# Optimization experiments

Measured on AMD Instinct MI355X. Metric: run time of the kernel, lower is better.

Reference implementation:

```python
import jax, jax.numpy as jnp
import numpy as np

N_NODES = 100000
N_EDGES = 1600000
NFEAT, NHID, NCLASS = 64, 128, 32


def _glorot(key, shape):
    fan_in, fan_out = shape[0], shape[1]
    lim = np.sqrt(6.0 / (fan_in + fan_out))
    return jax.random.uniform(key, shape, jnp.float32, -lim, lim)


def setup_inputs() -> dict:
    key = jax.random.key(0)
    ks = jax.random.split(key, 12)
    x = jax.random.normal(ks[0], (N_NODES, NFEAT), jnp.float32)
    edge_idx = jax.random.randint(ks[1], (2, N_EDGES), 0, N_NODES, jnp.int64)
    edge_weight = jax.random.uniform(ks[2], (N_EDGES,), jnp.float32)
    return {
        "x": x,
        "edge_idx": edge_idx,
        "edge_weight": edge_weight,
        # SAGEConv 1: out = mean_agg(x) @ Wl1 + b1 + x @ Wr1
        "Wl1": _glorot(ks[3], (NFEAT, NHID)),
        "Wr1": _glorot(ks[4], (NFEAT, NHID)),
        "b1": jnp.zeros((NHID,), jnp.float32),
        # SAGEConv 2
        "Wl2": _glorot(ks[5], (NHID, NHID)),
        "Wr2": _glorot(ks[6], (NHID, NHID)),
        "b2": jnp.zeros((NHID,), jnp.float32),
        # fc head: Linear(nhid, nclass) -> Linear(nclass, 1)
        "Wfc1": _glorot(ks[7], (NHID, NCLASS)),
        "bfc1": jnp.zeros((NCLASS,), jnp.float32),
        "Wfc2": _glorot(ks[8], (NCLASS, 1)),
        "bfc2": jnp.zeros((1,), jnp.float32),
    }


def _sage_conv(x, src, dst, Wl, Wr, b, n_nodes):
    # mean aggregation of source features at destination nodes
    msg_sum = jax.ops.segment_sum(x[src], dst, num_segments=n_nodes)  # [N, d]
    deg = jax.ops.segment_sum(jnp.ones((src.shape[0], 1), x.dtype), dst,
                              num_segments=n_nodes)                    # [N, 1]
    mean = msg_sum / jnp.maximum(deg, 1.0)
    return mean @ Wl + b + x @ Wr


def reference(x, edge_idx, edge_weight, Wl1, Wr1, b1, Wl2, Wr2, b2,
              Wfc1, bfc1, Wfc2, bfc2):
    n_nodes = x.shape[0]
    src, dst = edge_idx[0], edge_idx[1]
    # dropout is identity in eval mode (training=False)
    h = _sage_conv(x, src, dst, Wl1, Wr1, b1, n_nodes)   # [N, nhid]
    h = _sage_conv(h, src, dst, Wl2, Wr2, b2, n_nodes)   # [N, nhid]
    h = h @ Wfc1 + bfc1                                   # [N, nclass]
    out = h @ Wfc2 + bfc2                                 # [N, 1]
    return out
```

## Files before the change

kernel.cpp:

```cpp
#include <hip/hip_runtime.h>

#define S_SHIFT 8
#define S_NODES 256
#define NBKT    400
#define CAP     5120
#define CHUNK   8192
#define NREP    8
#define FTH     512
#define NDOTS   160

__global__ __launch_bounds__(FTH) void fused_kernel(
    const float* __restrict__ x,
    const int* __restrict__ src, const int* __restrict__ dst,
    int E, int N, int B, int nscat,
    int* __restrict__ cursor, unsigned* __restrict__ bucket,
    const float* __restrict__ Wl1, const float* __restrict__ Wr1, const float* __restrict__ b1,
    const float* __restrict__ Wl2, const float* __restrict__ Wr2, const float* __restrict__ b2,
    const float* __restrict__ Wfc1, const float* __restrict__ bfc1,
    const float* __restrict__ Wfc2, const float* __restrict__ bfc2,
    float* __restrict__ ga, float2* __restrict__ gbc, float* __restrict__ c01)
{
    __shared__ int hist[NBKT], lbase[NBKT], lcur[NBKT];
    __shared__ float wv[192], uu[128], vl2[128], vr2[128], w2[32];
    int t = threadIdx.x;
    int l = t & 63;
    int w = t >> 6;

    if ((int)blockIdx.x < nscat) {
        int e0 = blockIdx.x * CHUNK;
        int cnt = E - e0; if (cnt > CHUNK) cnt = CHUNK;
        for (int i = t; i < B; i += FTH) hist[i] = 0;
        __syncthreads();
        for (int i = t; i < cnt; i += FTH)
            atomicAdd(&hist[dst[e0 + i] >> S_SHIFT], 1);
        __syncthreads();
        for (int i = t; i < B; i += FTH) {
            lcur[i] = 0;
            if (hist[i] > 0) lbase[i] = atomicAdd(&cursor[i], hist[i]);
        }
        __syncthreads();
        for (int i = t; i < cnt; i += FTH) {
            int d = dst[e0 + i], s = src[e0 + i];
            int bb = d >> S_SHIFT;
            int off = atomicAdd(&lcur[bb], 1);
            bucket[(size_t)bb * CAP + (unsigned)(lbase[bb] + off)] =
                ((unsigned)s << S_SHIFT) | (unsigned)(d & (S_NODES - 1));
        }
    } else {
        if (t < 32) w2[t] = Wfc2[t];
        __syncthreads();
        for (int j = 0; j < 16; ++j) {
            int i = w + 8 * j;
            float p = (l < 32) ? Wfc1[i * 32 + l] * w2[l] : 0.f;
            for (int m = 16; m; m >>= 1) p += __shfl_xor(p, m);
            if (l == 0) uu[i] = p;
        }
        __syncthreads();
        for (int j = 0; j < 16; ++j) {
            int i = w + 8 * j;
            float ua = uu[l], ub = uu[64 + l];
            float pa = Wl2[i * 128 + l] * ua + Wl2[i * 128 + 64 + l] * ub;
            float pb = Wr2[i * 128 + l] * ua + Wr2[i * 128 + 64 + l] * ub;
            for (int m = 32; m; m >>= 1) { pa += __shfl_xor(pa, m); pb += __shfl_xor(pb, m); }
            if (l == 0) { vl2[i] = pa; vr2[i] = pb; }
        }
        __syncthreads();
        for (int j = 0; j < 8; ++j) {
            int i = w + 8 * j;
            float l1a = Wl1[i * 128 + l], l1b = Wl1[i * 128 + 64 + l];
            float r1a = Wr1[i * 128 + l], r1b = Wr1[i * 128 + 64 + l];
            float La = vl2[l], Lb = vl2[64 + l], Ra = vr2[l], Rb = vr2[64 + l];
            float pc = l1a * La + l1b * Lb;
            float pb = l1a * Ra + l1b * Rb + r1a * La + r1b * Lb;
            float pa = r1a * Ra + r1b * Rb;
            for (int m = 32; m; m >>= 1) {
                pa += __shfl_xor(pa, m); pb += __shfl_xor(pb, m); pc += __shfl_xor(pc, m);
            }
            if (l == 0) { wv[i] = pa; wv[64 + i] = pb; wv[128 + i] = pc; }
        }
        if ((int)blockIdx.x == nscat && w == 7) {
            float p0 = b1[l] * vr2[l] + b1[64 + l] * vr2[64 + l]
                     + b2[l] * uu[l] + b2[64 + l] * uu[64 + l];
            if (l < 32) p0 += bfc1[l] * w2[l];
            float p1 = b1[l] * vl2[l] + b1[64 + l] * vl2[64 + l];
            for (int m = 32; m; m >>= 1) { p0 += __shfl_xor(p0, m); p1 += __shfl_xor(p1, m); }
            if (l == 0) { c01[0] = p0 + bfc2[0]; c01[1] = p1; }
        }
        __syncthreads();

        int fp = l & 15, sub = l >> 4;
        float4 wa4 = ((const float4*)wv)[fp];
        float4 wb4 = ((const float4*)wv)[16 + fp];
        float4 wc4 = ((const float4*)wv)[32 + fp];
        const float4* x4 = (const float4*)x;
        int Q = (N + 3) >> 2;
        for (int qd = ((int)blockIdx.x - nscat) * 8 + w; qd < Q; qd += NDOTS * 8) {
            int node = qd * 4 + sub;
            float a = 0.f, b = 0.f, c = 0.f;
            if (node < N) {
                float4 v = x4[(size_t)node * 16 + fp];
                a = v.x * wa4.x + v.y * wa4.y + v.z * wa4.z + v.w * wa4.w;
                b = v.x * wb4.x + v.y * wb4.y + v.z * wb4.z + v.w * wb4.w;
                c = v.x * wc4.x + v.y * wc4.y + v.z * wc4.z + v.w * wc4.w;
            }
            for (int m = 8; m; m >>= 1) {
                a += __shfl_xor(a, m); b += __shfl_xor(b, m); c += __shfl_xor(c, m);
            }
            if (fp == 0 && node < N) { ga[node] = a; gbc[node] = make_float2(b, c); }
        }
    }
}

__global__ __launch_bounds__(512) void aggA_kernel(
    const unsigned* __restrict__ bucket, const int* __restrict__ cursor,
    const float2* __restrict__ gbc, const float* __restrict__ ga,
    const float* __restrict__ c01,
    float* __restrict__ q, float* __restrict__ t1, float* __restrict__ inv, int N)
{
    __shared__ float aB[NREP][S_NODES], aC[NREP][S_NODES];
    __shared__ int cnt[NREP][S_NODES];
    int t = threadIdx.x, b = blockIdx.x;
    int r = t >> 6;
    float* aBf = (float*)aB; float* aCf = (float*)aC; int* cnf = (int*)cnt;
    for (int i = t; i < NREP * S_NODES; i += 512) { aBf[i] = 0.f; aCf[i] = 0.f; cnf[i] = 0; }
    __syncthreads();
    int n = cursor[b];
    const unsigned* bp = bucket + (size_t)b * CAP;
    int n4 = n & ~3;
    for (int i = 4 * t; i < n4; i += 4 * 512) {
        uint4 e4 = *(const uint4*)(bp + i);
        float2 g0 = gbc[e4.x >> S_SHIFT];
        float2 g1 = gbc[e4.y >> S_SHIFT];
        float2 g2 = gbc[e4.z >> S_SHIFT];
        float2 g3 = gbc[e4.w >> S_SHIFT];
        int d0 = e4.x & (S_NODES - 1), d1 = e4.y & (S_NODES - 1);
        int d2 = e4.z & (S_NODES - 1), d3 = e4.w & (S_NODES - 1);
        atomicAdd(&aB[r][d0], g0.x); atomicAdd(&aC[r][d0], g0.y); atomicAdd(&cnt[r][d0], 1);
        atomicAdd(&aB[r][d1], g1.x); atomicAdd(&aC[r][d1], g1.y); atomicAdd(&cnt[r][d1], 1);
        atomicAdd(&aB[r][d2], g2.x); atomicAdd(&aC[r][d2], g2.y); atomicAdd(&cnt[r][d2], 1);
        atomicAdd(&aB[r][d3], g3.x); atomicAdd(&aC[r][d3], g3.y); atomicAdd(&cnt[r][d3], 1);
    }
    if (n4 + t < n) {
        unsigned uu = bp[n4 + t];
        float2 g = gbc[uu >> S_SHIFT];
        int dl = uu & (S_NODES - 1);
        atomicAdd(&aB[r][dl], g.x); atomicAdd(&aC[r][dl], g.y); atomicAdd(&cnt[r][dl], 1);
    }
    __syncthreads();
    if (t < S_NODES) {
        int node = (b << S_SHIFT) + t;
        if (node < N) {
            float sb = 0.f, sc = 0.f; int d = 0;
            #pragma unroll
            for (int k = 0; k < NREP; ++k) { sb += aB[k][t]; sc += aC[k][t]; d += cnt[k][t]; }
            float iv = 1.0f / ((d > 0) ? (float)d : 1.0f);
            inv[node] = iv;
            q[node]   = iv * sc;
            t1[node]  = ga[node] + iv * sb + c01[0] + (d > 0 ? c01[1] : 0.f);
        }
    }
}

__global__ __launch_bounds__(512) void aggB_kernel(
    const unsigned* __restrict__ bucket, const int* __restrict__ cursor,
    const float* __restrict__ q, const float* __restrict__ t1,
    const float* __restrict__ inv, float* __restrict__ out, int N)
{
    __shared__ float a2[NREP][S_NODES];
    int t = threadIdx.x, b = blockIdx.x;
    int r = t >> 6;
    float* a2f = (float*)a2;
    for (int i = t; i < NREP * S_NODES; i += 512) a2f[i] = 0.f;
    __syncthreads();
    int n = cursor[b];
    const unsigned* bp = bucket + (size_t)b * CAP;
    int n4 = n & ~3;
    for (int i = 4 * t; i < n4; i += 4 * 512) {
        uint4 e4 = *(const uint4*)(bp + i);
        float q0 = q[e4.x >> S_SHIFT], q1 = q[e4.y >> S_SHIFT];
        float q2 = q[e4.z >> S_SHIFT], q3 = q[e4.w >> S_SHIFT];
        atomicAdd(&a2[r][e4.x & (S_NODES - 1)], q0);
        atomicAdd(&a2[r][e4.y & (S_NODES - 1)], q1);
        atomicAdd(&a2[r][e4.z & (S_NODES - 1)], q2);
        atomicAdd(&a2[r][e4.w & (S_NODES - 1)], q3);
    }
    if (n4 + t < n) {
        unsigned uu = bp[n4 + t];
        atomicAdd(&a2[r][uu & (S_NODES - 1)], q[uu >> S_SHIFT]);
    }
    __syncthreads();
    if (t < S_NODES) {
        int node = (b << S_SHIFT) + t;
        if (node < N) {
            float s2 = 0.f;
            #pragma unroll
            for (int k = 0; k < NREP; ++k) s2 += a2[k][t];
            out[node] = t1[node] + inv[node] * s2;
        }
    }
}

extern "C" void kernel_launch(void* const* d_in, const int* in_sizes, int n_in,
                              void* d_out, int out_size, void* d_ws, size_t ws_size,
                              hipStream_t stream) {
    const float* x    = (const float*)d_in[0];
    const int*   eidx = (const int*)d_in[1];
    const float* Wl1  = (const float*)d_in[3];
    const float* Wr1  = (const float*)d_in[4];
    const float* b1   = (const float*)d_in[5];
    const float* Wl2  = (const float*)d_in[6];
    const float* Wr2  = (const float*)d_in[7];
    const float* b2   = (const float*)d_in[8];
    const float* Wfc1 = (const float*)d_in[9];
    const float* bfc1 = (const float*)d_in[10];
    const float* Wfc2 = (const float*)d_in[11];
    const float* bfc2 = (const float*)d_in[12];

    const int N = in_sizes[0] / 64;
    const int E = in_sizes[2];
    const int* src = eidx;
    const int* dst = eidx + E;
    const int B = (N + S_NODES - 1) / S_NODES;
    const int nscat = (E + CHUNK - 1) / CHUNK;

    char* ws = (char*)d_ws;
    int*      cursor = (int*)(ws);
    float*    c01    = (float*)(ws + 2048);
    float*    ga     = (float*)(ws + 4096);
    float*    q      = (float*)(ws + 4096 + (size_t)N * 4);
    float*    t1     = (float*)(ws + 4096 + (size_t)N * 8);
    float*    inv    = (float*)(ws + 4096 + (size_t)N * 12);
    float2*   gbc    = (float2*)(ws + 4096 + (size_t)N * 16);
    unsigned* bucket = (unsigned*)(ws + 4096 + (size_t)N * 24);

    hipMemsetAsync(cursor, 0, 2048, stream);

    fused_kernel<<<nscat + NDOTS, FTH, 0, stream>>>(
        x, src, dst, E, N, B, nscat, cursor, bucket,
        Wl1, Wr1, b1, Wl2, Wr2, b2, Wfc1, bfc1, Wfc2, bfc2,
        ga, gbc, c01);

    aggA_kernel<<<B, 512, 0, stream>>>(bucket, cursor, gbc, ga, c01, q, t1, inv, N);
    aggB_kernel<<<B, 512, 0, stream>>>(bucket, cursor, q, t1, inv, (float*)d_out, N);
}
```

Before: 168.7 us.

## Replace bucketed atomics with CSR counting sort in one cooperative kernel

```diff
diff --git a/kernel.cpp b/kernel.cpp
--- a/kernel.cpp
+++ b/kernel.cpp
@@ -1,74 +1,77 @@
 #include <hip/hip_runtime.h>
-
-#define S_SHIFT 8
-#define S_NODES 256
-#define NBKT    400
-#define CAP     5120
-#define CHUNK   8192
-#define NREP    8
-#define FTH     512
-#define NDOTS   160
-
-__global__ __launch_bounds__(FTH) void fused_kernel(
+#include <hip/hip_cooperative_groups.h>
+
+namespace cg = cooperative_groups;
+
+#define GRID   256
+#define TPB    512
+#define DCHUNK 16384
+
+__global__ __launch_bounds__(TPB) void mega_kernel(
     const float* __restrict__ x,
     const int* __restrict__ src, const int* __restrict__ dst,
-    int E, int N, int B, int nscat,
-    int* __restrict__ cursor, unsigned* __restrict__ bucket,
+    int E, int N, int nscat, int nscan,
+    int* __restrict__ deg, unsigned char* rank,
+    int* __restrict__ off_p, int* __restrict__ part, int* __restrict__ part2,
+    int* __restrict__ sorted,
     const float* __restrict__ Wl1, const float* __restrict__ Wr1, const float* __restrict__ b1,
     const float* __restrict__ Wl2, const float* __restrict__ Wr2, const float* __restrict__ b2,
     const float* __restrict__ Wfc1, const float* __restrict__ bfc1,
     const float* __restrict__ Wfc2, const float* __restrict__ bfc2,
-    float* __restrict__ ga, float2* __restrict__ gbc, float* __restrict__ c01)
+    float* __restrict__ ga, float2* __restrict__ gbc, float* __restrict__ c01,
+    float* q, float* t1, float* __restrict__ outp)
 {
-    __shared__ int hist[NBKT], lbase[NBKT], lcur[NBKT];
-    __shared__ float wv[192], uu[128], vl2[128], vr2[128], w2[32];
+    __shared__ __align__(16) float wv[192];
+    __shared__ float uu[128], vl2[128], vr2[128], w2[32];
+    __shared__ int scanbuf[TPB];
+    __shared__ int pbuf[256];
+    cg::grid_group grid = cg::this_grid();
     int t = threadIdx.x;
     int l = t & 63;
     int w = t >> 6;
-
-    if ((int)blockIdx.x < nscat) {
-        int e0 = blockIdx.x * CHUNK;
-        int cnt = E - e0; if (cnt > CHUNK) cnt = CHUNK;
-        for (int i = t; i < B; i += FTH) hist[i] = 0;
-        __syncthreads();
-        for (int i = t; i < cnt; i += FTH)
-            atomicAdd(&hist[dst[e0 + i] >> S_SHIFT], 1);
-        __syncthreads();
-        for (int i = t; i < B; i += FTH) {
-            lcur[i] = 0;
-            if (hist[i] > 0) lbase[i] = atomicAdd(&cursor[i], hist[i]);
-        }
-        __syncthreads();
-        for (int i = t; i < cnt; i += FTH) {
-            int d = dst[e0 + i], s = src[e0 + i];
-            int bb = d >> S_SHIFT;
-            int off = atomicAdd(&lcur[bb], 1);
-            bucket[(size_t)bb * CAP + (unsigned)(lbase[bb] + off)] =
-                ((unsigned)s << S_SHIFT) | (unsigned)(d & (S_NODES - 1));
-        }
+    int bid = blockIdx.x;
+
+    if (bid < nscat) {
+        int e0 = bid * DCHUNK;
+        int cnt = E - e0; if (cnt > DCHUNK) cnt = DCHUNK;
+        int i = t;
+        for (; i + 3 * TPB < cnt; i += 4 * TPB) {
+            int d0 = dst[e0 + i], d1 = dst[e0 + i + TPB];
+            int d2 = dst[e0 + i + 2 * TPB], d3 = dst[e0 + i + 3 * TPB];
+            int r0 = atomicAdd(&deg[d0], 1);
+            int r1 = atomicAdd(&deg[d1], 1);
+            int r2 = atomicAdd(&deg[d2], 1);
+            int r3 = atomicAdd(&deg[d3], 1);
+            rank[e0 + i]           = (unsigned char)r0;
+            rank[e0 + i + TPB]     = (unsigned char)r1;
+            rank[e0 + i + 2 * TPB] = (unsigned char)r2;
+            rank[e0 + i + 3 * TPB] = (unsigned char)r3;
+        }
+        for (; i < cnt; i += TPB)
+            rank[e0 + i] = (unsigned char)atomicAdd(&deg[dst[e0 + i]], 1);
     } else {
         if (t < 32) w2[t] = Wfc2[t];
         __syncthreads();
         for (int j = 0; j < 16; ++j) {
-            int i = w + 8 * j;
-            float p = (l < 32) ? Wfc1[i * 32 + l] * w2[l] : 0.f;
+            int ii = w + 8 * j;
+            float p = (l < 32) ? Wfc1[ii * 32 + l] * w2[l] : 0.f;
             for (int m = 16; m; m >>= 1) p += __shfl_xor(p, m);
-            if (l == 0) uu[i] = p;
+            if (l == 0) uu[ii] = p;
         }
         __syncthreads();
         for (int j = 0; j < 16; ++j) {
-            int i = w + 8 * j;
+            int ii = w + 8 * j;
             float ua = uu[l], ub = uu[64 + l];
-            float pa = Wl2[i * 128 + l] * ua + Wl2[i * 128 + 64 + l] * ub;
-            float pb = Wr2[i * 128 + l] * ua + Wr2[i * 128 + 64 + l] * ub;
+            float pa = Wl2[ii * 128 + l] * ua + Wl2[ii * 128 + 64 + l] * ub;
+            float pb = Wr2[ii * 128 + l] * ua + Wr2[ii * 128 + 64 + l] * ub;
             for (int m = 32; m; m >>= 1) { pa += __shfl_xor(pa, m); pb += __shfl_xor(pb, m); }
-            if (l == 0) { vl2[i] = pa; vr2[i] = pb; }
+            if (l == 0) { vl2[ii] = pa; vr2[ii] = pb; }
         }
         __syncthreads();
         for (int j = 0; j < 8; ++j) {
-            int i = w + 8 * j;
-            float l1a = Wl1[i * 128 + l], l1b = Wl1[i * 128 + 64 + l];
-            float r1a = Wr1[i * 128 + l], r1b = Wr1[i * 128 + 64 + l];
+            int ii = w + 8 * j;
+            float l1a = Wl1[ii * 128 + l], l1b = Wl1[ii * 128 + 64 + l];
+            float r1a = Wr1[ii * 128 + l], r1b = Wr1[ii * 128 + 64 + l];
             float La = vl2[l], Lb = vl2[64 + l], Ra = vr2[l], Rb = vr2[64 + l];
             float pc = l1a * La + l1b * Lb;
             float pb = l1a * Ra + l1b * Rb + r1a * La + r1b * Lb;
@@ -76,9 +79,9 @@
             for (int m = 32; m; m >>= 1) {
                 pa += __shfl_xor(pa, m); pb += __shfl_xor(pb, m); pc += __shfl_xor(pc, m);
             }
-            if (l == 0) { wv[i] = pa; wv[64 + i] = pb; wv[128 + i] = pc; }
-        }
-        if ((int)blockIdx.x == nscat && w == 7) {
+            if (l == 0) { wv[ii] = pa; wv[64 + ii] = pb; wv[128 + ii] = pc; }
+        }
+        if (bid == nscat && w == 7) {
             float p0 = b1[l] * vr2[l] + b1[64 + l] * vr2[64 + l]
                      + b2[l] * uu[l] + b2[64 + l] * uu[64 + l];
             if (l < 32) p0 += bfc1[l] * w2[l];
@@ -94,7 +97,10 @@
         float4 wc4 = ((const float4*)wv)[32 + fp];
         const float4* x4 = (const float4*)x;
         int Q = (N + 3) >> 2;
-        for (int qd = ((int)blockIdx.x - nscat) * 8 + w; qd < Q; qd += NDOTS * 8) {
+        int ndot = GRID - nscat;
+        int wid = (bid - nscat) * 8 + w;
+        int stride = ndot * 8;
+        for (int qd = wid; qd < Q; qd += stride) {
             int node = qd * 4 + sub;
             float a = 0.f, b = 0.f, c = 0.f;
             if (node < N) {
@@ -109,93 +115,91 @@
             if (fp == 0 && node < N) { ga[node] = a; gbc[node] = make_float2(b, c); }
         }
     }
-}
-
-__global__ __launch_bounds__(512) void aggA_kernel(
-    const unsigned* __restrict__ bucket, const int* __restrict__ cursor,
-    const float2* __restrict__ gbc, const float* __restrict__ ga,
-    const float* __restrict__ c01,
-    float* __restrict__ q, float* __restrict__ t1, float* __restrict__ inv, int N)
-{
-    __shared__ float aB[NREP][S_NODES], aC[NREP][S_NODES];
-    __shared__ int cnt[NREP][S_NODES];
-    int t = threadIdx.x, b = blockIdx.x;
-    int r = t >> 6;
-    float* aBf = (float*)aB; float* aCf = (float*)aC; int* cnf = (int*)cnt;
-    for (int i = t; i < NREP * S_NODES; i += 512) { aBf[i] = 0.f; aCf[i] = 0.f; cnf[i] = 0; }
-    __syncthreads();
-    int n = cursor[b];
-    const unsigned* bp = bucket + (size_t)b * CAP;
-    int n4 = n & ~3;
-    for (int i = 4 * t; i < n4; i += 4 * 512) {
-        uint4 e4 = *(const uint4*)(bp + i);
-        float2 g0 = gbc[e4.x >> S_SHIFT];
-        float2 g1 = gbc[e4.y >> S_SHIFT];
-        float2 g2 = gbc[e4.z >> S_SHIFT];
-        float2 g3 = gbc[e4.w >> S_SHIFT];
-        int d0 = e4.x & (S_NODES - 1), d1 = e4.y & (S_NODES - 1);
-        int d2 = e4.z & (S_NODES - 1), d3 = e4.w & (S_NODES - 1);
-        atomicAdd(&aB[r][d0], g0.x); atomicAdd(&aC[r][d0], g0.y); atomicAdd(&cnt[r][d0], 1);
-        atomicAdd(&aB[r][d1], g1.x); atomicAdd(&aC[r][d1], g1.y); atomicAdd(&cnt[r][d1], 1);
-        atomicAdd(&aB[r][d2], g2.x); atomicAdd(&aC[r][d2], g2.y); atomicAdd(&cnt[r][d2], 1);
-        atomicAdd(&aB[r][d3], g3.x); atomicAdd(&aC[r][d3], g3.y); atomicAdd(&cnt[r][d3], 1);
-    }
-    if (n4 + t < n) {
-        unsigned uu = bp[n4 + t];
-        float2 g = gbc[uu >> S_SHIFT];
-        int dl = uu & (S_NODES - 1);
-        atomicAdd(&aB[r][dl], g.x); atomicAdd(&aC[r][dl], g.y); atomicAdd(&cnt[r][dl], 1);
-    }
-    __syncthreads();
-    if (t < S_NODES) {
-        int node = (b << S_SHIFT) + t;
+    __threadfence();
+    grid.sync();
+
+    if (bid < nscan) {
+        int node = bid * TPB + t;
+        int val = (node < N) ? deg[node] : 0;
+        scanbuf[t] = val;
+        __syncthreads();
+        for (int d2 = 1; d2 < TPB; d2 <<= 1) {
+            int xx = (t >= d2) ? scanbuf[t - d2] : 0;
+            __syncthreads();
+            scanbuf[t] += xx;
+            __syncthreads();
+        }
+        int incl = scanbuf[t];
+        if (node < N) off_p[node] = incl - val;
+        if (t == TPB - 1) part[bid] = incl;
+    }
+    __threadfence();
+    grid.sync();
+
+    if (bid == 0) {
+        int val = (t < nscan) ? part[t] : 0;
+        if (t < 256) pbuf[t] = val;
+        __syncthreads();
+        for (int d2 = 1; d2 < 256; d2 <<= 1) {
+            int xx = (t >= d2 && t < 256) ? pbuf[t - d2] : 0;
+            __syncthreads();
+            if (t < 256) pbuf[t] += xx;
+            __syncthreads();
+        }
+        if (t < nscan) part2[t] = pbuf[t] - val;
+    }
+    __threadfence();
+    grid.sync();
+
+    {
+        int stride = GRID * TPB;
+        for (int e = bid * TPB + t; e < E; e += stride) {
+            int d = dst[e];
+            int pos = off_p[d] + part2[d >> 9] + (int)rank[e];
+            sorted[pos] = src[e];
+        }
+    }
+    __threadfence();
+    grid.sync();
+
+    {
+        int node = bid * TPB + t;
         if (node < N) {
-            float sb = 0.f, sc = 0.f; int d = 0;
-            #pragma unroll
-            for (int k = 0; k < NREP; ++k) { sb += aB[k][t]; sc += aC[k][t]; d += cnt[k][t]; }
-            float iv = 1.0f / ((d > 0) ? (float)d : 1.0f);
-            inv[node] = iv;
-            q[node]   = iv * sc;
-            t1[node]  = ga[node] + iv * sb + c01[0] + (d > 0 ? c01[1] : 0.f);
-        }
-    }
-}
-
-__global__ __launch_bounds__(512) void aggB_kernel(
-    const unsigned* __restrict__ bucket, const int* __restrict__ cursor,
-    const float* __restrict__ q, const float* __restrict__ t1,
-    const float* __restrict__ inv, float* __restrict__ out, int N)
-{
-    __shared__ float a2[NREP][S_NODES];
-    int t = threadIdx.x, b = blockIdx.x;
-    int r = t >> 6;
-    float* a2f = (float*)a2;
-    for (int i = t; i < NREP * S_NODES; i += 512) a2f[i] = 0.f;
-    __syncthreads();
-    int n = cursor[b];
-    const unsigned* bp = bucket + (size_t)b * CAP;
-    int n4 = n & ~3;
-    for (int i = 4 * t; i < n4; i += 4 * 512) {
-        uint4 e4 = *(const uint4*)(bp + i);
-        float q0 = q[e4.x >> S_SHIFT], q1 = q[e4.y >> S_SHIFT];
-        float q2 = q[e4.z >> S_SHIFT], q3 = q[e4.w >> S_SHIFT];
-        atomicAdd(&a2[r][e4.x & (S_NODES - 1)], q0);
-        atomicAdd(&a2[r][e4.y & (S_NODES - 1)], q1);
-        atomicAdd(&a2[r][e4.z & (S_NODES - 1)], q2);
-        atomicAdd(&a2[r][e4.w & (S_NODES - 1)], q3);
-    }
-    if (n4 + t < n) {
-        unsigned uu = bp[n4 + t];
-        atomicAdd(&a2[r][uu & (S_NODES - 1)], q[uu >> S_SHIFT]);
-    }
-    __syncthreads();
-    if (t < S_NODES) {
-        int node = (b << S_SHIFT) + t;
+            int dg = deg[node];
+            int base = off_p[node] + part2[node >> 9];
+            float sb = 0.f, sc = 0.f;
+            int k = 0;
+            for (; k + 4 <= dg; k += 4) {
+                int s0 = sorted[base + k],     s1 = sorted[base + k + 1];
+                int s2 = sorted[base + k + 2], s3 = sorted[base + k + 3];
+                float2 g0 = gbc[s0], g1 = gbc[s1], g2 = gbc[s2], g3 = gbc[s3];
+                sb += (g0.x + g1.x) + (g2.x + g3.x);
+                sc += (g0.y + g1.y) + (g2.y + g3.y);
+            }
+            for (; k < dg; ++k) { float2 g = gbc[sorted[base + k]]; sb += g.x; sc += g.y; }
+            float iv = 1.0f / ((dg > 0) ? (float)dg : 1.0f);
+            q[node]  = iv * sc;
+            t1[node] = ga[node] + iv * sb + c01[0] + (dg > 0 ? c01[1] : 0.f);
+        }
+    }
+    __threadfence();
+    grid.sync();
+
+    {
+        int node = bid * TPB + t;
         if (node < N) {
+            int dg = deg[node];
+            int base = off_p[node] + part2[node >> 9];
             float s2 = 0.f;
-            #pragma unroll
-            for (int k = 0; k < NREP; ++k) s2 += a2[k][t];
-            out[node] = t1[node] + inv[node] * s2;
+            int k = 0;
+            for (; k + 4 <= dg; k += 4) {
+                float q0 = q[sorted[base + k]],     q1 = q[sorted[base + k + 1]];
+                float q2 = q[sorted[base + k + 2]], q3 = q[sorted[base + k + 3]];
+                s2 += (q0 + q1) + (q2 + q3);
+            }
+            for (; k < dg; ++k) s2 += q[sorted[base + k]];
+            float iv = 1.0f / ((dg > 0) ? (float)dg : 1.0f);
+            outp[node] = t1[node] + iv * s2;
         }
     }
 }
@@ -220,26 +224,35 @@
     const int E = in_sizes[2];
     const int* src = eidx;
     const int* dst = eidx + E;
-    const int B = (N + S_NODES - 1) / S_NODES;
-    const int nscat = (E + CHUNK - 1) / CHUNK;
+    const int nscat = (E + DCHUNK - 1) / DCHUNK;
+    const int nscan = (N + TPB - 1) / TPB;
 
     char* ws = (char*)d_ws;
-    int*      cursor = (int*)(ws);
-    float*    c01    = (float*)(ws + 2048);
-    float*    ga     = (float*)(ws + 4096);
-    float*    q      = (float*)(ws + 4096 + (size_t)N * 4);
-    float*    t1     = (float*)(ws + 4096 + (size_t)N * 8);
-    float*    inv    = (float*)(ws + 4096 + (size_t)N * 12);
-    float2*   gbc    = (float2*)(ws + 4096 + (size_t)N * 16);
-    unsigned* bucket = (unsigned*)(ws + 4096 + (size_t)N * 24);
-
-    hipMemsetAsync(cursor, 0, 2048, stream);
-
-    fused_kernel<<<nscat + NDOTS, FTH, 0, stream>>>(
-        x, src, dst, E, N, B, nscat, cursor, bucket,
-        Wl1, Wr1, b1, Wl2, Wr2, b2, Wfc1, bfc1, Wfc2, bfc2,
-        ga, gbc, c01);
-
-    aggA_kernel<<<B, 512, 0, stream>>>(bucket, cursor, gbc, ga, c01, q, t1, inv, N);
-    aggB_kernel<<<B, 512, 0, stream>>>(bucket, cursor, q, t1, inv, (float*)d_out, N);
+    size_t o = 0;
+    auto take = [&](size_t bytes) { char* p = ws + o; o += (bytes + 127) & ~(size_t)127; return p; };
+    int*           deg    = (int*)take((size_t)N * 4);
+    unsigned char* rank   = (unsigned char*)take((size_t)E);
+    int*           off_p  = (int*)take((size_t)N * 4);
+    int*           part   = (int*)take(1024);
+    int*           part2  = (int*)take(1024);
+    float*         c01    = (float*)take(64);
+    float*         ga     = (float*)take((size_t)N * 4);
+    float2*        gbc    = (float2*)take((size_t)N * 8);
+    int*           sorted = (int*)take((size_t)E * 4);
+    float* q  = (float*)rank;
+    float* t1 = ((float*)rank) + N;
+    float* outp = (float*)d_out;
+
+    hipMemsetAsync(deg, 0, (size_t)N * 4, stream);
+
+    int E_ = E, N_ = N, nscat_ = nscat, nscan_ = nscan;
+    void* args[] = {
+        (void*)&x, (void*)&src, (void*)&dst, (void*)&E_, (void*)&N_, (void*)&nscat_, (void*)&nscan_,
+        (void*)&deg, (void*)&rank, (void*)&off_p, (void*)&part, (void*)&part2, (void*)&sorted,
+        (void*)&Wl1, (void*)&Wr1, (void*)&b1, (void*)&Wl2, (void*)&Wr2, (void*)&b2,
+        (void*)&Wfc1, (void*)&bfc1, (void*)&Wfc2, (void*)&bfc2,
+        (void*)&ga, (void*)&gbc, (void*)&c01, (void*)&q, (void*)&t1, (void*)&outp
+    };
+    hipLaunchCooperativeKernel(reinterpret_cast<void*>(mega_kernel),
+                               dim3(GRID), dim3(TPB), args, 0, stream);
 }
```

Result: slower. 609.8 us (+261.5%).
